# Optimization experiments

Hardware: AMD Instinct MI355X
Metric: run time of the kernel (lower is better)

## Reference

```python
import jax, jax.numpy as jnp
import numpy as np

T, H, N, D = 4096, 16, 16, 64


def setup_inputs() -> dict:
    key = jax.random.key(0)
    ks = jax.random.split(key, 8)
    x = jax.random.normal(ks[0], (T, H, D), dtype=jnp.float32)
    dt = jax.random.uniform(ks[1], (T, H), dtype=jnp.float32) * 0.1  # small positive timesteps
    B = jax.random.normal(ks[2], (T, H, N), dtype=jnp.float32)
    C = jax.random.normal(ks[3], (T, H, N), dtype=jnp.float32)
    mask = jax.random.randint(ks[4], (T,), 0, 2).astype(jnp.float32)  # reset flags in {0,1}
    initial_carry = jax.random.normal(ks[5], (H, N, D), dtype=jnp.float32)
    log_decay = jax.random.normal(ks[6], (H,), dtype=jnp.float32) * 0.1
    skip_weight = jnp.ones((H, D), dtype=jnp.float32)
    return {"x": x, "dt": dt, "B": B, "C": C, "mask": mask,
            "initial_carry": initial_carry, "log_decay": log_decay,
            "skip_weight": skip_weight}


def _binary_operator(q_i, q_j):
    # elementwise; broadcasting replaces the original per-time vmap
    a_i, b_i, c_i = q_i
    a_j, b_j, c_j = q_j
    a_out = a_j * a_i * (1.0 - c_j) + a_j * c_j
    b_out = (a_j * b_i + b_j) * (1.0 - c_j) + b_j * c_j
    c_out = c_i * (1.0 - c_j) + c_j
    return (a_out, b_out, c_out)


def reference(x, dt, B, C, mask, initial_carry, log_decay, skip_weight):
    num_heads = dt.shape[1]
    decay_rate = -jnp.exp(log_decay)                        # [H]
    decay_factor = jnp.exp(dt * decay_rate[None, :])        # [T,H]
    decay_factor = decay_factor[:, :, None, None]           # [T,H,1,1]
    decay_factor = jnp.concatenate(
        [jnp.ones((1, num_heads, 1, 1), dtype=decay_factor.dtype), decay_factor], axis=0)
    driving_input = jnp.einsum('th,thn,thd->thnd', dt, B, x)  # [T,H,N,D]
    driving_input = jnp.concatenate([initial_carry[None, ...], driving_input], axis=0)
    m = jnp.concatenate([jnp.zeros((1,), dtype=mask.dtype), mask])
    m = m[:, None, None, None]                              # [T+1,1,1,1]
    _, hidden_states, _ = jax.lax.associative_scan(
        _binary_operator, (decay_factor, driving_input, m))
    next_carry = hidden_states[-1]                          # [H,N,D]
    valid_states = hidden_states[1:]                        # [T,H,N,D]
    output = jnp.einsum('thn,thnd->thd', C, valid_states)   # [T,H,D]
    output = output + skip_weight[None, :, :] * x
    return (next_carry, output)
```

## Files before the change

### kernel.cpp

```cpp
#include <hip/hip_runtime.h>

#define T_LEN 4096
#define H 16
#define N 16
#define D 64
#define NC 256
#define CL (T_LEN / NC)
#define CPB 4
#define HND (H * N * D)

static __device__ __forceinline__ unsigned short f2bf(float f) {
    union { float f; unsigned u; } v; v.f = f;
    unsigned r = (v.u + 0x7fffu + ((v.u >> 16) & 1u)) >> 16;
    return (unsigned short)r;
}
static __device__ __forceinline__ float bf2f(unsigned short s) {
    union { unsigned u; float f; } v; v.u = ((unsigned)s) << 16;
    return v.f;
}

__global__ __launch_bounds__(256)
void k1_local(const float* __restrict__ x, const float* __restrict__ dt,
              const float* __restrict__ B, const float* __restrict__ mask,
              const float* __restrict__ log_decay,
              unsigned short* __restrict__ Lb, float* __restrict__ Pbuf,
              float* __restrict__ Abuf) {
    const int cq = blockIdx.x, h = blockIdx.y;
    const int tid = threadIdx.x;
    const int w = tid >> 6, d = tid & 63;
    const int c = cq * CPB + w;
    const int t00 = cq * CPB * CL;
    const float rate = -__expf(log_decay[h]);

    __shared__ float Bs[CPB * CL * N];
    __shared__ float As[CPB * CL];
    {
        const float4* Bg = (const float4*)B;
        const int j = tid;
        const int row = j >> 2, off = j & 3;
        const int t = t00 + row;
        const float dtv = dt[t * H + h];
        float4 bv = Bg[(t * H + h) * (N / 4) + off];
        bv.x *= dtv; bv.y *= dtv; bv.z *= dtv; bv.w *= dtv;
        ((float4*)Bs)[j] = bv;
        if (off == 0) {
            const float av = (1.f - mask[t]) * __expf(dtv * rate);
            As[row] = av;
            Abuf[h * T_LEN + t] = av;
        }
    }
    __syncthreads();

    float s[N];
#pragma unroll
    for (int n = 0; n < N; ++n) s[n] = 0.f;
    float P = 1.f;
    const int t0 = c * CL;

#pragma unroll
    for (int ss = 0; ss < CL; ++ss) {
        const float a  = As[w * CL + ss];
        const float xv = x[((t0 + ss) * H + h) * D + d];
        P *= a;
        const float4* Br4 = (const float4*)(Bs + (w * CL + ss) * N);
#pragma unroll
        for (int q = 0; q < 4; ++q) {
            const float4 bv = Br4[q];
            s[4*q+0] = a * s[4*q+0] + bv.x * xv;
            s[4*q+1] = a * s[4*q+1] + bv.y * xv;
            s[4*q+2] = a * s[4*q+2] + bv.z * xv;
            s[4*q+3] = a * s[4*q+3] + bv.w * xv;
        }
    }

    unsigned short* Lp = Lb + ((size_t)(c * H + h) * N) * D + d;
#pragma unroll
    for (int n = 0; n < N; ++n) Lp[n * D] = f2bf(s[n]);
    if (d == 0) Pbuf[h * NC + c] = P;
}

__global__ __launch_bounds__(64)
void k2_combine(const float* __restrict__ initial_carry,
                unsigned short* __restrict__ LE, const float* __restrict__ Pbuf,
                float* __restrict__ next_carry) {
    const int idx = blockIdx.x * 64 + threadIdx.x;
    const int h = blockIdx.x >> 4;
    float carry = initial_carry[idx];

#pragma unroll 1
    for (int r = 0; r < NC / 128; ++r) {
        float l[128];
#pragma unroll
        for (int k = 0; k < 128; ++k)
            l[k] = bf2f(LE[(size_t)(r * 128 + k) * HND + idx]);
#pragma unroll
        for (int k = 0; k < 128; ++k) {
            const float p = Pbuf[h * NC + r * 128 + k];
            LE[(size_t)(r * 128 + k) * HND + idx] = f2bf(carry);
            carry = p * carry + l[k];
        }
    }
    next_carry[idx] = carry;
}

__global__ __launch_bounds__(256)
void k3_scan(const float* __restrict__ x, const float* __restrict__ dt,
             const float* __restrict__ B, const float* __restrict__ C,
             const float* __restrict__ skip_weight,
             const float* __restrict__ Abuf,
             const unsigned short* __restrict__ Eb, float* __restrict__ out) {
    const int cq = blockIdx.x, h = blockIdx.y;
    const int tid = threadIdx.x;
    const int w = tid >> 6, d = tid & 63;
    const int c = cq * CPB + w;
    const int t00 = cq * CPB * CL;

    __shared__ float Bs[CPB * CL * N], Cs[CPB * CL * N];
    __shared__ float As[CPB * CL];
    {
        const float4* Bg = (const float4*)B;
        const float4* Cg = (const float4*)C;
        const int j = tid;
        const int row = j >> 2, off = j & 3;
        const int t = t00 + row;
        const float dtv = dt[t * H + h];
        float4 bv = Bg[(t * H + h) * (N / 4) + off];
        bv.x *= dtv; bv.y *= dtv; bv.z *= dtv; bv.w *= dtv;
        ((float4*)Bs)[j] = bv;
        ((float4*)Cs)[j] = Cg[(t * H + h) * (N / 4) + off];
        if (tid < CPB * CL) As[tid] = Abuf[h * T_LEN + t00 + tid];
    }
    __syncthreads();

    float s[N];
    const unsigned short* Ep = Eb + ((size_t)(c * H + h) * N) * D + d;
#pragma unroll
    for (int n = 0; n < N; ++n) s[n] = bf2f(Ep[n * D]);

    const float swv = skip_weight[h * D + d];
    const int t0 = c * CL;
#pragma unroll
    for (int ss = 0; ss < CL; ++ss) {
        const int t = t0 + ss;
        const float a  = As[w * CL + ss];
        const float xv = x[(t * H + h) * D + d];
        float acc = swv * xv;
        const float4* Br4 = (const float4*)(Bs + (w * CL + ss) * N);
        const float4* Cr4 = (const float4*)(Cs + (w * CL + ss) * N);
#pragma unroll
        for (int q = 0; q < 4; ++q) {
            const float4 bv = Br4[q];
            const float4 cv = Cr4[q];
            s[4*q+0] = a * s[4*q+0] + bv.x * xv;  acc += cv.x * s[4*q+0];
            s[4*q+1] = a * s[4*q+1] + bv.y * xv;  acc += cv.y * s[4*q+1];
            s[4*q+2] = a * s[4*q+2] + bv.z * xv;  acc += cv.z * s[4*q+2];
            s[4*q+3] = a * s[4*q+3] + bv.w * xv;  acc += cv.w * s[4*q+3];
        }
        __builtin_nontemporal_store(acc, &out[(t * H + h) * D + d]);
    }
}

extern "C" void kernel_launch(void* const* d_in, const int* in_sizes, int n_in,
                              void* d_out, int out_size, void* d_ws, size_t ws_size,
                              hipStream_t stream) {
    const float* x    = (const float*)d_in[0];
    const float* dt   = (const float*)d_in[1];
    const float* B    = (const float*)d_in[2];
    const float* C    = (const float*)d_in[3];
    const float* mask = (const float*)d_in[4];
    const float* ic   = (const float*)d_in[5];
    const float* ld   = (const float*)d_in[6];
    const float* sw   = (const float*)d_in[7];
    float* out = (float*)d_out;

    float* Pbuf = (float*)d_ws;
    float* Abuf = (float*)((char*)d_ws + 16384);
    unsigned short* Lb = (unsigned short*)((char*)d_ws + 16384 + T_LEN * H * 4);

    dim3 grid(NC / CPB, H), block(256);
    k1_local<<<grid, block, 0, stream>>>(x, dt, B, mask, ld, Lb, Pbuf, Abuf);
    k2_combine<<<dim3(HND / 64), dim3(64), 0, stream>>>(ic, Lb, Pbuf, out);
    k3_scan<<<grid, block, 0, stream>>>(x, dt, B, C, sw, Abuf, Lb, out + HND);
}
```

Before: 34.51 us.

## Transpose chunk-state buffer to d-major layout with packed bf16 vector accesses

The per-chunk bf16 state buffer changes from [c][h][n][d] to [c][h][d][n] order. k1 and k3 now write and read each thread's 16 states as two 16-byte vectors instead of 16 strided 2-byte accesses. k2 handles two adjacent n values per thread with 32-bit packed loads and stores, so it launches half as many blocks. The aim is fewer, wider memory transactions. In exchange, k2 has half the threads for the sequential combine, which lowers parallelism there, and the k1/k3 uint4 accesses are strided across lanes.

```diff
diff --git a/kernel.cpp b/kernel.cpp
--- a/kernel.cpp
+++ b/kernel.cpp
@@ -18,6 +18,7 @@
     union { unsigned u; float f; } v; v.u = ((unsigned)s) << 16;
     return v.f;
 }
+
 
 __global__ __launch_bounds__(256)
 void k1_local(const float* __restrict__ x, const float* __restrict__ dt,
@@ -73,9 +74,13 @@
         }
     }
 
-    unsigned short* Lp = Lb + ((size_t)(c * H + h) * N) * D + d;
-#pragma unroll
-    for (int n = 0; n < N; ++n) Lp[n * D] = f2bf(s[n]);
+    unsigned pk[8];
+#pragma unroll
+    for (int i = 0; i < 8; ++i)
+        pk[i] = (unsigned)f2bf(s[2*i]) | ((unsigned)f2bf(s[2*i+1]) << 16);
+    uint4* Lp = (uint4*)(Lb + ((size_t)((c * H + h) * D + d)) * N);
+    Lp[0] = make_uint4(pk[0], pk[1], pk[2], pk[3]);
+    Lp[1] = make_uint4(pk[4], pk[5], pk[6], pk[7]);
     if (d == 0) Pbuf[h * NC + c] = P;
 }
 
@@ -83,24 +88,32 @@
 void k2_combine(const float* __restrict__ initial_carry,
                 unsigned short* __restrict__ LE, const float* __restrict__ Pbuf,
                 float* __restrict__ next_carry) {
-    const int idx = blockIdx.x * 64 + threadIdx.x;
-    const int h = blockIdx.x >> 4;
-    float carry = initial_carry[idx];
+    const int idx2 = blockIdx.x * 64 + threadIdx.x;
+    const int iN = idx2 * 2;
+    const int n0 = iN & 15, d = (iN >> 4) & 63;
+    const int h = blockIdx.x >> 3;
+    unsigned* LEu = (unsigned*)LE;
+
+    float c0 = initial_carry[h * 1024 + n0 * 64 + d];
+    float c1 = initial_carry[h * 1024 + (n0 + 1) * 64 + d];
 
 #pragma unroll 1
     for (int r = 0; r < NC / 128; ++r) {
-        float l[128];
+        unsigned l[128];
 #pragma unroll
         for (int k = 0; k < 128; ++k)
-            l[k] = bf2f(LE[(size_t)(r * 128 + k) * HND + idx]);
+            l[k] = LEu[(size_t)(r * 128 + k) * (HND / 2) + idx2];
 #pragma unroll
         for (int k = 0; k < 128; ++k) {
             const float p = Pbuf[h * NC + r * 128 + k];
-            LE[(size_t)(r * 128 + k) * HND + idx] = f2bf(carry);
-            carry = p * carry + l[k];
-        }
-    }
-    next_carry[idx] = carry;
+            LEu[(size_t)(r * 128 + k) * (HND / 2) + idx2] =
+                (unsigned)f2bf(c0) | ((unsigned)f2bf(c1) << 16);
+            c0 = p * c0 + bf2f((unsigned short)(l[k] & 0xffffu));
+            c1 = p * c1 + bf2f((unsigned short)(l[k] >> 16));
+        }
+    }
+    next_carry[h * 1024 + n0 * 64 + d] = c0;
+    next_carry[h * 1024 + (n0 + 1) * 64 + d] = c1;
 }
 
 __global__ __launch_bounds__(256)
@@ -133,9 +146,16 @@
     __syncthreads();
 
     float s[N];
-    const unsigned short* Ep = Eb + ((size_t)(c * H + h) * N) * D + d;
-#pragma unroll
-    for (int n = 0; n < N; ++n) s[n] = bf2f(Ep[n * D]);
+    {
+        const uint4* Ep = (const uint4*)(Eb + ((size_t)((c * H + h) * D + d)) * N);
+        const uint4 e0 = Ep[0], e1 = Ep[1];
+        const unsigned ew[8] = {e0.x, e0.y, e0.z, e0.w, e1.x, e1.y, e1.z, e1.w};
+#pragma unroll
+        for (int i = 0; i < 8; ++i) {
+            s[2*i]   = bf2f((unsigned short)(ew[i] & 0xffffu));
+            s[2*i+1] = bf2f((unsigned short)(ew[i] >> 16));
+        }
+    }
 
     const float swv = skip_weight[h * D + d];
     const int t0 = c * CL;
@@ -179,6 +199,6 @@
 
     dim3 grid(NC / CPB, H), block(256);
     k1_local<<<grid, block, 0, stream>>>(x, dt, B, mask, ld, Lb, Pbuf, Abuf);
-    k2_combine<<<dim3(HND / 64), dim3(64), 0, stream>>>(ic, Lb, Pbuf, out);
+    k2_combine<<<dim3(HND / 128), dim3(64), 0, stream>>>(ic, Lb, Pbuf, out);
     k3_scan<<<grid, block, 0, stream>>>(x, dt, B, C, sw, Abuf, Lb, out + HND);
 }
```

Result: slower. 41.46 us (+20.1%).
